# Kernel tuning notes

Hardware: AMD Instinct MI355X
Metric: run time of the kernel (lower is better)

## Reference

```python
import jax, jax.numpy as jnp
import numpy as np

B, S, D, E, TOP_K = 2, 1024, 1024, 8, 2
H = 4 * D  # FFN hidden


def setup_inputs() -> dict:
    key = jax.random.key(0)
    ks = jax.random.split(key, 12)
    sc = 0.02
    return {
        "x": jax.random.normal(ks[0], (B, S, D), jnp.float32),
        # gate: nn.Linear(D, E) -> weight [E, D], bias [E]; routing bias param [E]
        "Wg": jax.random.normal(ks[1], (E, D), jnp.float32) * sc,
        "bg": jnp.zeros((E,), jnp.float32),
        "bias": jnp.zeros((E,), jnp.float32),
        # routed experts: stacked Linear(D,4D) and Linear(4D,D) weights (torch layout [out,in])
        "W1": jax.random.normal(ks[2], (E, H, D), jnp.float32) * sc,
        "b1": jnp.zeros((E, H), jnp.float32),
        "W2": jax.random.normal(ks[3], (E, D, H), jnp.float32) * sc,
        "b2": jnp.zeros((E, D), jnp.float32),
        # shared expert
        "Ws1": jax.random.normal(ks[4], (H, D), jnp.float32) * sc,
        "bs1": jnp.zeros((H,), jnp.float32),
        "Ws2": jax.random.normal(ks[5], (D, H), jnp.float32) * sc,
        "bs2": jnp.zeros((D,), jnp.float32),
    }


def reference(x, Wg, bg, bias, W1, b1, W2, b2, Ws1, bs1, Ws2, bs2):
    b, s, d = x.shape
    xf = x.reshape(-1, d)  # [T, D]
    T = xf.shape[0]

    # sigmoid gating with learnable routing bias
    scores = jax.nn.sigmoid(xf @ Wg.T + bg + bias)          # [T, E]
    top_scores, top_idx = jax.lax.top_k(scores, TOP_K)      # [T, K]

    # per-token per-expert combine weights (zero for unselected experts)
    weights = jnp.zeros((T, E), scores.dtype)
    weights = weights.at[jnp.arange(T)[:, None], top_idx].add(top_scores)  # [T, E]

    # dense grouped expert MLP (mask-and-matmul form of gather-GEMM-scatter)
    h = jax.nn.gelu(jnp.einsum("td,ehd->teh", xf, W1) + b1, approximate=False)  # [T, E, H]
    eo = jnp.einsum("teh,edh->ted", h, W2) + b2                                  # [T, E, D]
    combined = jnp.einsum("ted,te->td", eo, weights)                             # [T, D]

    # shared expert applied to every token
    shared = jax.nn.gelu(xf @ Ws1.T + bs1, approximate=False) @ Ws2.T + bs2      # [T, D]

    return (shared + combined).reshape(b, s, d)
```

## Files before the change

kernel.cpp:

```cpp
#include <hip/hip_runtime.h>
#include <hip/hip_bf16.h>
#include <math.h>

#define NTOK 2048
#define DDIM 1024
#define HDIM 4096
#define NEXP 8
#define NROWS (3 * NTOK)
#define KSPLIT2 2

typedef __bf16 bf16x8 __attribute__((ext_vector_type(8)));
typedef float f32x4 __attribute__((ext_vector_type(4)));
typedef __attribute__((address_space(1))) char as1_char;
typedef __attribute__((address_space(3))) char as3_char;

__device__ __forceinline__ void async16(const void* g, void* l) {
  __builtin_amdgcn_global_load_lds((as1_char*)g, (as3_char*)l, 16, 0, 0);
}

__device__ __forceinline__ float gelu_fast(float v) {
  const float x = v * 0.70710678118654752f;
  const float ax = fabsf(x);
  const float t = __builtin_amdgcn_rcpf(1.0f + 0.3275911f * ax);
  float p = 1.061405429f;
  p = p * t - 1.453152027f;
  p = p * t + 1.421413741f;
  p = p * t - 0.284496736f;
  p = p * t + 0.254829592f;
  const float y = 1.0f - p * t * __expf(-ax * ax);
  const float erfv = copysignf(y, x);
  return 0.5f * v * (1.0f + erfv);
}

__global__ void __launch_bounds__(256) cvt_bf16(const float* __restrict__ in,
                                                __hip_bfloat16* __restrict__ out) {
  const size_t i = ((size_t)blockIdx.x * 256 + threadIdx.x) * 8;
  const float4 a = *(const float4*)(in + i);
  const float4 b = *(const float4*)(in + i + 4);
  union { __hip_bfloat16 h[8]; uint4 u; } p;
  p.h[0] = __float2bfloat16(a.x); p.h[1] = __float2bfloat16(a.y);
  p.h[2] = __float2bfloat16(a.z); p.h[3] = __float2bfloat16(a.w);
  p.h[4] = __float2bfloat16(b.x); p.h[5] = __float2bfloat16(b.y);
  p.h[6] = __float2bfloat16(b.z); p.h[7] = __float2bfloat16(b.w);
  *(uint4*)(out + i) = p.u;
}

__global__ void moe_zero_out(float* __restrict__ a) {
  a[(size_t)blockIdx.x * 256 + threadIdx.x] = 0.f;
}
__global__ void moe_zero_misc(int* counts) {
  if (threadIdx.x < NEXP) counts[threadIdx.x] = 0;
}

__device__ __forceinline__ void gemm_core(const char* ga0, const char* ga1,
                                          const char* gb0, const char* gb1,
                                          char* sm, int Kbytes, int tid,
                                          f32x4 acc[4][4]) {
  const int w = tid >> 6, l = tid & 63;
  const int lr = l & 15, quad = l >> 4;
  const int wr = w >> 1, wc = w & 1;
  const int swz = (lr >> 1) & 3;
  const int aoff = (wr * 64 + lr) * 64 + ((quad ^ swz) * 16);
  const int boff = 8192 + (wc * 64 + lr) * 64 + ((quad ^ swz) * 16);
  const int niter = Kbytes >> 6;

  auto stage = [&](int it, int buf) {
    char* base = sm + buf * 16384 + w * 1024;
    const int kb = it * 64;
    async16(ga0 + kb, base);
    async16(ga1 + kb, base + 4096);
    async16(gb0 + kb, base + 8192);
    async16(gb1 + kb, base + 12288);
  };

  stage(0, 0);
  stage(1, 1);
  int cur = 0, nxt = 2;
  for (int i = 0; i < niter; ++i) {
    if (i + 2 < niter) {
      stage(i + 2, nxt);
      __builtin_amdgcn_s_waitcnt(0x0F78);
    } else if (i + 1 < niter) {
      __builtin_amdgcn_s_waitcnt(0x0F74);
    } else {
      __builtin_amdgcn_s_waitcnt(0x0F70);
    }
    __builtin_amdgcn_s_barrier();
    const char* rb = sm + cur * 16384;
    bf16x8 av[4], bv[4];
#pragma unroll
    for (int i2 = 0; i2 < 4; ++i2) av[i2] = *(const bf16x8*)(rb + aoff + i2 * 1024);
#pragma unroll
    for (int j = 0; j < 4; ++j) bv[j] = *(const bf16x8*)(rb + boff + j * 1024);
#pragma unroll
    for (int i2 = 0; i2 < 4; ++i2)
#pragma unroll
      for (int j = 0; j < 4; ++j)
        acc[i2][j] = __builtin_amdgcn_mfma_f32_16x16x32_bf16(av[i2], bv[j], acc[i2][j], 0, 0, 0);
    __builtin_amdgcn_s_barrier();
    cur = (cur == 2) ? 0 : cur + 1;
    nxt = (nxt == 2) ? 0 : nxt + 1;
  }
}

__device__ __forceinline__ int stage_colb(int l) {
  return (((l & 3) ^ ((l >> 3) & 3)) * 16);
}

__global__ void __launch_bounds__(64) moe_gate(
    const float* __restrict__ x, const float* __restrict__ Wg,
    const float* __restrict__ bg, const float* __restrict__ bias,
    int* __restrict__ counts, int* __restrict__ topk_idx,
    float* __restrict__ topk_w, int* __restrict__ slot) {
  const int t = blockIdx.x, lane = threadIdx.x;
  float xv[16];
#pragma unroll
  for (int q = 0; q < 16; ++q) xv[q] = x[(size_t)t * DDIM + q * 64 + lane];
  float sc[NEXP];
#pragma unroll
  for (int e = 0; e < NEXP; ++e) {
    float s = 0.f;
#pragma unroll
    for (int q = 0; q < 16; ++q) s += xv[q] * Wg[(size_t)e * DDIM + q * 64 + lane];
#pragma unroll
    for (int o = 32; o > 0; o >>= 1) s += __shfl_xor(s, o, 64);
    sc[e] = 1.0f / (1.0f + expf(-(s + bg[e] + bias[e])));
  }
  if (lane == 0) {
    int k0 = 0;
    for (int e = 1; e < NEXP; ++e)
      if (sc[e] > sc[k0]) k0 = e;
    int k1 = (k0 == 0) ? 1 : 0;
    for (int e = 0; e < NEXP; ++e) {
      if (e == k0) continue;
      if (sc[e] > sc[k1]) k1 = e;
    }
    topk_idx[t * 2 + 0] = k0;
    topk_idx[t * 2 + 1] = k1;
    topk_w[t * 2 + 0] = sc[k0];
    topk_w[t * 2 + 1] = sc[k1];
    slot[t * 2 + 0] = atomicAdd(&counts[k0], 1);
    slot[t * 2 + 1] = atomicAdd(&counts[k1], 1);
  }
}

__global__ void moe_scan(const int* __restrict__ counts, int* __restrict__ offsets) {
  if (threadIdx.x == 0) {
    int s = 0;
    for (int e = 0; e < NEXP; ++e) { offsets[e] = s; s += counts[e]; }
    offsets[NEXP] = s;
  }
}

__global__ void moe_scatter(const int* __restrict__ topk_idx, const float* __restrict__ topk_w,
                            const int* __restrict__ slot, const int* __restrict__ offsets,
                            int* __restrict__ row_token, float* __restrict__ row_w) {
  const int t = blockIdx.x * blockDim.x + threadIdx.x;
  if (t >= NTOK) return;
#pragma unroll
  for (int k = 0; k < 2; ++k) {
    const int e = topk_idx[t * 2 + k];
    const int rg = offsets[e] + slot[t * 2 + k];
    row_token[rg] = t;
    row_w[rg] = topk_w[t * 2 + k];
  }
  row_token[2 * NTOK + t] = t;
  row_w[2 * NTOK + t] = 1.0f;
}

__global__ void __launch_bounds__(256) moe_gemm1(
    const __hip_bfloat16* __restrict__ xbf, const __hip_bfloat16* __restrict__ W1bf,
    const float* __restrict__ b1, const __hip_bfloat16* __restrict__ Ws1bf,
    const float* __restrict__ bs1, const int* __restrict__ counts,
    const int* __restrict__ offsets, const int* __restrict__ row_token,
    __hip_bfloat16* __restrict__ h1) {
  __shared__ alignas(16) char sm[49152];
  const int e = blockIdx.z, mt = blockIdx.y, nt = blockIdx.x;
  const int cnt = (e < NEXP) ? counts[e] : NTOK;
  if (mt * 128 >= cnt) return;
  const int off = (e < NEXP) ? offsets[e] : 2 * NTOK;
  const __hip_bfloat16* Bw = (e < NEXP) ? (W1bf + (size_t)e * HDIM * DDIM) : Ws1bf;
  const float* bb = (e < NEXP) ? (b1 + e * HDIM) : bs1;

  const int tid = threadIdx.x;
  const int w = tid >> 6, l = tid & 63;
  const int mrow = w * 16 + (l >> 2);
  const int colb = stage_colb(l);

  const int r0 = mt * 128 + mrow, r1 = r0 + 64;
  const int c0 = (r0 < cnt) ? r0 : (cnt - 1);
  const int c1 = (r1 < cnt) ? r1 : (cnt - 1);
  const int t0 = row_token[off + c0];
  const int t1 = row_token[off + c1];
  const char* ga0 = (const char*)xbf + (size_t)t0 * (DDIM * 2) + colb;
  const char* ga1 = (const char*)xbf + (size_t)t1 * (DDIM * 2) + colb;
  const char* gb0 = (const char*)Bw + (size_t)(nt * 128 + mrow) * (DDIM * 2) + colb;
  const char* gb1 = (const char*)Bw + (size_t)(nt * 128 + mrow + 64) * (DDIM * 2) + colb;

  f32x4 acc[4][4] = {};
  gemm_core(ga0, ga1, gb0, gb1, sm, DDIM * 2, tid, acc);

  const int lr = l & 15, quad = l >> 4, wr = w >> 1, wc = w & 1;
#pragma unroll
  for (int i = 0; i < 4; ++i) {
#pragma unroll
    for (int r = 0; r < 4; ++r) {
      const int rowe = mt * 128 + wr * 64 + i * 16 + quad * 4 + r;
      if (rowe >= cnt) continue;
      const size_t orow = (size_t)(off + rowe) * HDIM;
#pragma unroll
      for (int j = 0; j < 4; ++j) {
        const int h = nt * 128 + wc * 64 + j * 16 + lr;
        const float v = acc[i][j][r] + bb[h];
        h1[orow + h] = __float2bfloat16(gelu_fast(v));
      }
    }
  }
}

__global__ void __launch_bounds__(256) moe_gemm2(
    const __hip_bfloat16* __restrict__ h1, const __hip_bfloat16* __restrict__ W2bf,
    const float* __restrict__ b2, const __hip_bfloat16* __restrict__ Ws2bf,
    const float* __restrict__ bs2, const int* __restrict__ counts,
    const int* __restrict__ offsets, const int* __restrict__ row_token,
    const float* __restrict__ row_w, float* __restrict__ out) {
  __shared__ alignas(16) char sm[49152];
  const int e = blockIdx.z, mt = blockIdx.y;
  const int nt = blockIdx.x & (DDIM / 128 - 1);
  const int kc = blockIdx.x >> 3;
  const int cnt = (e < NEXP) ? counts[e] : NTOK;
  if (mt * 128 >= cnt) return;
  const int off = (e < NEXP) ? offsets[e] : 2 * NTOK;
  const __hip_bfloat16* Bw = (e < NEXP) ? (W2bf + (size_t)e * DDIM * HDIM) : Ws2bf;
  const float* bb = (e < NEXP) ? (b2 + e * DDIM) : bs2;

  const int tid = threadIdx.x;
  const int w = tid >> 6, l = tid & 63;
  const int mrow = w * 16 + (l >> 2);
  const int colb = stage_colb(l);
  const int KB = (HDIM * 2) / KSPLIT2;
  const size_t kofs = (size_t)kc * KB;

  const char* ga0 = (const char*)h1 + (size_t)(off + mt * 128 + mrow) * (HDIM * 2) + kofs + colb;
  const char* ga1 = (const char*)h1 + (size_t)(off + mt * 128 + mrow + 64) * (HDIM * 2) + kofs + colb;
  const char* gb0 = (const char*)Bw + (size_t)(nt * 128 + mrow) * (HDIM * 2) + kofs + colb;
  const char* gb1 = (const char*)Bw + (size_t)(nt * 128 + mrow + 64) * (HDIM * 2) + kofs + colb;

  f32x4 acc[4][4] = {};
  gemm_core(ga0, ga1, gb0, gb1, sm, KB, tid, acc);

  const int lr = l & 15, quad = l >> 4, wr = w >> 1, wc = w & 1;
#pragma unroll
  for (int i = 0; i < 4; ++i) {
#pragma unroll
    for (int r = 0; r < 4; ++r) {
      const int rowe = mt * 128 + wr * 64 + i * 16 + quad * 4 + r;
      if (rowe >= cnt) continue;
      const int rg = off + rowe;
      const int tok = row_token[rg];
      const float wt = row_w[rg];
#pragma unroll
      for (int j = 0; j < 4; ++j) {
        const int d = nt * 128 + wc * 64 + j * 16 + lr;
        const float base = (kc == 0) ? bb[d] : 0.f;
        atomicAdd(&out[(size_t)tok * DDIM + d], wt * (acc[i][j][r] + base));
      }
    }
  }
}

extern "C" void kernel_launch(void* const* d_in, const int* in_sizes, int n_in,
                              void* d_out, int out_size, void* d_ws, size_t ws_size,
                              hipStream_t stream) {
  (void)in_sizes; (void)n_in; (void)out_size; (void)ws_size;
  const float* x    = (const float*)d_in[0];
  const float* Wg   = (const float*)d_in[1];
  const float* bg   = (const float*)d_in[2];
  const float* bias = (const float*)d_in[3];
  const float* W1   = (const float*)d_in[4];
  const float* b1   = (const float*)d_in[5];
  const float* W2   = (const float*)d_in[6];
  const float* b2   = (const float*)d_in[7];
  const float* Ws1  = (const float*)d_in[8];
  const float* bs1  = (const float*)d_in[9];
  const float* Ws2  = (const float*)d_in[10];
  const float* bs2  = (const float*)d_in[11];
  float* out = (float*)d_out;

  char* ws = (char*)d_ws;
  size_t cur = 0;
  auto take = [&](size_t b) -> void* {
    void* p = ws + cur;
    cur += (b + 255) & ~(size_t)255;
    return p;
  };
  int* counts    = (int*)take(NEXP * 4);
  int* offsets   = (int*)take((NEXP + 1) * 4);
  int* topk_idx  = (int*)take(NTOK * 2 * 4);
  float* topk_w  = (float*)take(NTOK * 2 * 4);
  int* slot      = (int*)take(NTOK * 2 * 4);
  int* row_token = (int*)take(NROWS * 4);
  float* row_w   = (float*)take(NROWS * 4);
  __hip_bfloat16* xbf   = (__hip_bfloat16*)take((size_t)NTOK * DDIM * 2);
  __hip_bfloat16* W1bf  = (__hip_bfloat16*)take((size_t)NEXP * HDIM * DDIM * 2);
  __hip_bfloat16* W2bf  = (__hip_bfloat16*)take((size_t)NEXP * DDIM * HDIM * 2);
  __hip_bfloat16* Ws1bf = (__hip_bfloat16*)take((size_t)HDIM * DDIM * 2);
  __hip_bfloat16* Ws2bf = (__hip_bfloat16*)take((size_t)DDIM * HDIM * 2);
  __hip_bfloat16* h1    = (__hip_bfloat16*)take((size_t)(NROWS + 64) * HDIM * 2);

  cvt_bf16<<<(NTOK * DDIM) / 2048, 256, 0, stream>>>(x, xbf);
  cvt_bf16<<<(NEXP * HDIM * DDIM) / 2048, 256, 0, stream>>>(W1, W1bf);
  cvt_bf16<<<(NEXP * DDIM * HDIM) / 2048, 256, 0, stream>>>(W2, W2bf);
  cvt_bf16<<<(HDIM * DDIM) / 2048, 256, 0, stream>>>(Ws1, Ws1bf);
  cvt_bf16<<<(DDIM * HDIM) / 2048, 256, 0, stream>>>(Ws2, Ws2bf);

  moe_zero_misc<<<1, 64, 0, stream>>>(counts);
  moe_zero_out<<<(NTOK * DDIM) / 256, 256, 0, stream>>>(out);
  moe_gate<<<NTOK, 64, 0, stream>>>(x, Wg, bg, bias, counts, topk_idx, topk_w, slot);
  moe_scan<<<1, 1, 0, stream>>>(counts, offsets);
  moe_scatter<<<NTOK / 256, 256, 0, stream>>>(topk_idx, topk_w, slot, offsets, row_token, row_w);

  dim3 g1(HDIM / 128, NTOK / 128, NEXP + 1);
  moe_gemm1<<<g1, 256, 0, stream>>>(xbf, W1bf, b1, Ws1bf, bs1, counts, offsets, row_token, h1);

  dim3 g2(KSPLIT2 * (DDIM / 128), NTOK / 128, NEXP + 1);
  moe_gemm2<<<g2, 256, 0, stream>>>(h1, W2bf, b2, Ws2bf, bs2, counts, offsets, row_token, row_w, out);
}
```

Before: 365.8 us.

## Widen GEMM tiles to 128x256 with double buffering instead of triple

The shared GEMM core now computes a 128x256 output tile per block. Each wave owns a 64-column slab and all 128 rows, holding 8x4 MFMA accumulators. The pipeline drops from three LDS buffers to two 24KB buffers. Per-wave global staging pointers are passed as arrays, and both expert GEMM grids are halved along N. The aim is higher arithmetic intensity per LDS load and fewer blocks re-reading the A operand, at the cost of more accumulator registers (lower occupancy) and shallower prefetch.

Result: slower. 442.4 us (+21.0%).

```diff
diff --git a/kernel.cpp b/kernel.cpp
--- a/kernel.cpp
+++ b/kernel.cpp
@@ -52,54 +52,50 @@
   if (threadIdx.x < NEXP) counts[threadIdx.x] = 0;
 }
 
-__device__ __forceinline__ void gemm_core(const char* ga0, const char* ga1,
-                                          const char* gb0, const char* gb1,
+__device__ __forceinline__ void gemm_core(const char* const* gA,
+                                          const char* const* gB,
                                           char* sm, int Kbytes, int tid,
-                                          f32x4 acc[4][4]) {
+                                          f32x4 acc[8][4]) {
   const int w = tid >> 6, l = tid & 63;
   const int lr = l & 15, quad = l >> 4;
-  const int wr = w >> 1, wc = w & 1;
-  const int swz = (lr >> 1) & 3;
-  const int aoff = (wr * 64 + lr) * 64 + ((quad ^ swz) * 16);
-  const int boff = 8192 + (wc * 64 + lr) * 64 + ((quad ^ swz) * 16);
+  const int swz16 = (quad ^ ((lr >> 1) & 3)) * 16;
   const int niter = Kbytes >> 6;
 
   auto stage = [&](int it, int buf) {
-    char* base = sm + buf * 16384 + w * 1024;
+    char* base = sm + buf * 24576;
     const int kb = it * 64;
-    async16(ga0 + kb, base);
-    async16(ga1 + kb, base + 4096);
-    async16(gb0 + kb, base + 8192);
-    async16(gb1 + kb, base + 12288);
+    async16(gA[0] + kb, base + w * 2048);
+    async16(gA[1] + kb, base + w * 2048 + 1024);
+    async16(gB[0] + kb, base + 8192 + w * 4096);
+    async16(gB[1] + kb, base + 8192 + w * 4096 + 1024);
+    async16(gB[2] + kb, base + 8192 + w * 4096 + 2048);
+    async16(gB[3] + kb, base + 8192 + w * 4096 + 3072);
   };
 
   stage(0, 0);
-  stage(1, 1);
-  int cur = 0, nxt = 2;
   for (int i = 0; i < niter; ++i) {
-    if (i + 2 < niter) {
-      stage(i + 2, nxt);
-      __builtin_amdgcn_s_waitcnt(0x0F78);
-    } else if (i + 1 < niter) {
-      __builtin_amdgcn_s_waitcnt(0x0F74);
+    const int cur = i & 1;
+    if (i + 1 < niter) {
+      stage(i + 1, cur ^ 1);
+      __builtin_amdgcn_s_waitcnt(0x0F76);
     } else {
       __builtin_amdgcn_s_waitcnt(0x0F70);
     }
     __builtin_amdgcn_s_barrier();
-    const char* rb = sm + cur * 16384;
-    bf16x8 av[4], bv[4];
-#pragma unroll
-    for (int i2 = 0; i2 < 4; ++i2) av[i2] = *(const bf16x8*)(rb + aoff + i2 * 1024);
-#pragma unroll
-    for (int j = 0; j < 4; ++j) bv[j] = *(const bf16x8*)(rb + boff + j * 1024);
-#pragma unroll
-    for (int i2 = 0; i2 < 4; ++i2)
+    const char* rb = sm + cur * 24576;
+    bf16x8 av[8], bv[4];
+#pragma unroll
+    for (int i2 = 0; i2 < 8; ++i2)
+      av[i2] = *(const bf16x8*)(rb + (i2 * 16 + lr) * 64 + swz16);
+#pragma unroll
+    for (int j = 0; j < 4; ++j)
+      bv[j] = *(const bf16x8*)(rb + 8192 + (w * 64 + j * 16 + lr) * 64 + swz16);
+#pragma unroll
+    for (int i2 = 0; i2 < 8; ++i2)
 #pragma unroll
       for (int j = 0; j < 4; ++j)
         acc[i2][j] = __builtin_amdgcn_mfma_f32_16x16x32_bf16(av[i2], bv[j], acc[i2][j], 0, 0, 0);
     __builtin_amdgcn_s_barrier();
-    cur = (cur == 2) ? 0 : cur + 1;
-    nxt = (nxt == 2) ? 0 : nxt + 1;
   }
 }
 
@@ -184,33 +180,38 @@
 
   const int tid = threadIdx.x;
   const int w = tid >> 6, l = tid & 63;
-  const int mrow = w * 16 + (l >> 2);
+  const int rl = l >> 2;
   const int colb = stage_colb(l);
 
-  const int r0 = mt * 128 + mrow, r1 = r0 + 64;
-  const int c0 = (r0 < cnt) ? r0 : (cnt - 1);
-  const int c1 = (r1 < cnt) ? r1 : (cnt - 1);
-  const int t0 = row_token[off + c0];
-  const int t1 = row_token[off + c1];
-  const char* ga0 = (const char*)xbf + (size_t)t0 * (DDIM * 2) + colb;
-  const char* ga1 = (const char*)xbf + (size_t)t1 * (DDIM * 2) + colb;
-  const char* gb0 = (const char*)Bw + (size_t)(nt * 128 + mrow) * (DDIM * 2) + colb;
-  const char* gb1 = (const char*)Bw + (size_t)(nt * 128 + mrow + 64) * (DDIM * 2) + colb;
-
-  f32x4 acc[4][4] = {};
-  gemm_core(ga0, ga1, gb0, gb1, sm, DDIM * 2, tid, acc);
-
-  const int lr = l & 15, quad = l >> 4, wr = w >> 1, wc = w & 1;
-#pragma unroll
-  for (int i = 0; i < 4; ++i) {
+  const char* ga[2];
+#pragma unroll
+  for (int q = 0; q < 2; ++q) {
+    const int r0 = mt * 128 + w * 32 + q * 16 + rl;
+    const int c0 = (r0 < cnt) ? r0 : (cnt - 1);
+    const int t0 = row_token[off + c0];
+    ga[q] = (const char*)xbf + (size_t)t0 * (DDIM * 2) + colb;
+  }
+  const char* gb[4];
+#pragma unroll
+  for (int q = 0; q < 4; ++q) {
+    const int br = nt * 256 + w * 64 + q * 16 + rl;
+    gb[q] = (const char*)Bw + (size_t)br * (DDIM * 2) + colb;
+  }
+
+  f32x4 acc[8][4] = {};
+  gemm_core(ga, gb, sm, DDIM * 2, tid, acc);
+
+  const int lr = l & 15, quad = l >> 4;
+#pragma unroll
+  for (int i = 0; i < 8; ++i) {
 #pragma unroll
     for (int r = 0; r < 4; ++r) {
-      const int rowe = mt * 128 + wr * 64 + i * 16 + quad * 4 + r;
+      const int rowe = mt * 128 + i * 16 + quad * 4 + r;
       if (rowe >= cnt) continue;
       const size_t orow = (size_t)(off + rowe) * HDIM;
 #pragma unroll
       for (int j = 0; j < 4; ++j) {
-        const int h = nt * 128 + wc * 64 + j * 16 + lr;
+        const int h = nt * 256 + w * 64 + j * 16 + lr;
         const float v = acc[i][j][r] + bb[h];
         h1[orow + h] = __float2bfloat16(gelu_fast(v));
       }
@@ -226,8 +227,8 @@
     const float* __restrict__ row_w, float* __restrict__ out) {
   __shared__ alignas(16) char sm[49152];
   const int e = blockIdx.z, mt = blockIdx.y;
-  const int nt = blockIdx.x & (DDIM / 128 - 1);
-  const int kc = blockIdx.x >> 3;
+  const int nt = blockIdx.x & (DDIM / 256 - 1);
+  const int kc = blockIdx.x >> 2;
   const int cnt = (e < NEXP) ? counts[e] : NTOK;
   if (mt * 128 >= cnt) return;
   const int off = (e < NEXP) ? offsets[e] : 2 * NTOK;
@@ -236,32 +237,40 @@
 
   const int tid = threadIdx.x;
   const int w = tid >> 6, l = tid & 63;
-  const int mrow = w * 16 + (l >> 2);
+  const int rl = l >> 2;
   const int colb = stage_colb(l);
   const int KB = (HDIM * 2) / KSPLIT2;
   const size_t kofs = (size_t)kc * KB;
 
-  const char* ga0 = (const char*)h1 + (size_t)(off + mt * 128 + mrow) * (HDIM * 2) + kofs + colb;
-  const char* ga1 = (const char*)h1 + (size_t)(off + mt * 128 + mrow + 64) * (HDIM * 2) + kofs + colb;
-  const char* gb0 = (const char*)Bw + (size_t)(nt * 128 + mrow) * (HDIM * 2) + kofs + colb;
-  const char* gb1 = (const char*)Bw + (size_t)(nt * 128 + mrow + 64) * (HDIM * 2) + kofs + colb;
-
-  f32x4 acc[4][4] = {};
-  gemm_core(ga0, ga1, gb0, gb1, sm, KB, tid, acc);
-
-  const int lr = l & 15, quad = l >> 4, wr = w >> 1, wc = w & 1;
-#pragma unroll
-  for (int i = 0; i < 4; ++i) {
+  const char* ga[2];
+#pragma unroll
+  for (int q = 0; q < 2; ++q) {
+    const int ar = mt * 128 + w * 32 + q * 16 + rl;
+    ga[q] = (const char*)h1 + (size_t)(off + ar) * (HDIM * 2) + kofs + colb;
+  }
+  const char* gb[4];
+#pragma unroll
+  for (int q = 0; q < 4; ++q) {
+    const int br = nt * 256 + w * 64 + q * 16 + rl;
+    gb[q] = (const char*)Bw + (size_t)br * (HDIM * 2) + kofs + colb;
+  }
+
+  f32x4 acc[8][4] = {};
+  gemm_core(ga, gb, sm, KB, tid, acc);
+
+  const int lr = l & 15, quad = l >> 4;
+#pragma unroll
+  for (int i = 0; i < 8; ++i) {
 #pragma unroll
     for (int r = 0; r < 4; ++r) {
-      const int rowe = mt * 128 + wr * 64 + i * 16 + quad * 4 + r;
+      const int rowe = mt * 128 + i * 16 + quad * 4 + r;
       if (rowe >= cnt) continue;
       const int rg = off + rowe;
       const int tok = row_token[rg];
       const float wt = row_w[rg];
 #pragma unroll
       for (int j = 0; j < 4; ++j) {
-        const int d = nt * 128 + wc * 64 + j * 16 + lr;
+        const int d = nt * 256 + w * 64 + j * 16 + lr;
         const float base = (kc == 0) ? bb[d] : 0.f;
         atomicAdd(&out[(size_t)tok * DDIM + d], wt * (acc[i][j][r] + base));
       }
@@ -320,9 +329,9 @@
   moe_scan<<<1, 1, 0, stream>>>(counts, offsets);
   moe_scatter<<<NTOK / 256, 256, 0, stream>>>(topk_idx, topk_w, slot, offsets, row_token, row_w);
 
-  dim3 g1(HDIM / 128, NTOK / 128, NEXP + 1);
+  dim3 g1(HDIM / 256, NTOK / 128, NEXP + 1);
   moe_gemm1<<<g1, 256, 0, stream>>>(xbf, W1bf, b1, Ws1bf, bs1, counts, offsets, row_token, h1);
 
-  dim3 g2(KSPLIT2 * (DDIM / 128), NTOK / 128, NEXP + 1);
+  dim3 g2(KSPLIT2 * (DDIM / 256), NTOK / 128, NEXP + 1);
   moe_gemm2<<<g2, 256, 0, stream>>>(h1, W2bf, b2, Ws2bf, bs2, counts, offsets, row_token, row_w, out);
 }
```

## Load fp32 weights directly in GEMMs and convert to bf16 in-register

Applied to the files above, without the earlier changes.

Removes the separate fp32-to-bf16 conversion passes over W1, W2, Ws1 and Ws2. The GEMM kernels now stage fp32 weight tiles into LDS with an 8-way swizzle and convert them to bf16 after the LDS read. This saves a full read and write of the weights per call, but doubles the weight bytes moved per GEMM tile and LDS use grows to 72KB, which may reduce occupancy. It also folds the counts zeroing into the x conversion kernel to drop one launch.

After: 362.7 us. Within noise of the previous version (-0.8%).

```diff
diff --git a/kernel.cpp b/kernel.cpp
--- a/kernel.cpp
+++ b/kernel.cpp
@@ -32,8 +32,10 @@
   return 0.5f * v * (1.0f + erfv);
 }
 
-__global__ void __launch_bounds__(256) cvt_bf16(const float* __restrict__ in,
-                                                __hip_bfloat16* __restrict__ out) {
+__global__ void __launch_bounds__(256) cvt_x(const float* __restrict__ in,
+                                             __hip_bfloat16* __restrict__ out,
+                                             int* __restrict__ counts) {
+  if (blockIdx.x == 0 && threadIdx.x < NEXP) counts[threadIdx.x] = 0;
   const size_t i = ((size_t)blockIdx.x * 256 + threadIdx.x) * 8;
   const float4 a = *(const float4*)(in + i);
   const float4 b = *(const float4*)(in + i + 4);
@@ -48,29 +50,28 @@
 __global__ void moe_zero_out(float* __restrict__ a) {
   a[(size_t)blockIdx.x * 256 + threadIdx.x] = 0.f;
 }
-__global__ void moe_zero_misc(int* counts) {
-  if (threadIdx.x < NEXP) counts[threadIdx.x] = 0;
-}
 
 __device__ __forceinline__ void gemm_core(const char* ga0, const char* ga1,
-                                          const char* gb0, const char* gb1,
-                                          char* sm, int Kbytes, int tid,
+                                          const char* const gb[4],
+                                          char* sm, int niter, int tid,
                                           f32x4 acc[4][4]) {
   const int w = tid >> 6, l = tid & 63;
   const int lr = l & 15, quad = l >> 4;
   const int wr = w >> 1, wc = w & 1;
-  const int swz = (lr >> 1) & 3;
-  const int aoff = (wr * 64 + lr) * 64 + ((quad ^ swz) * 16);
-  const int boff = 8192 + (wc * 64 + lr) * 64 + ((quad ^ swz) * 16);
-  const int niter = Kbytes >> 6;
+  const int swz4 = (lr >> 1) & 3;
+  const int aoff = (wr * 64 + lr) * 64 + ((quad ^ swz4) * 16);
+  const int s8 = lr & 7;
+  const int bslot0 = ((2 * quad) ^ s8) * 16;
+  const int bslot1 = ((2 * quad + 1) ^ s8) * 16;
+  const int bbase = 8192 + (wc * 64 + lr) * 128;
 
   auto stage = [&](int it, int buf) {
-    char* base = sm + buf * 16384 + w * 1024;
-    const int kb = it * 64;
-    async16(ga0 + kb, base);
-    async16(ga1 + kb, base + 4096);
-    async16(gb0 + kb, base + 8192);
-    async16(gb1 + kb, base + 12288);
+    char* base = sm + buf * 24576;
+    async16(ga0 + it * 64, base + w * 1024);
+    async16(ga1 + it * 64, base + 4096 + w * 1024);
+#pragma unroll
+    for (int q = 0; q < 4; ++q)
+      async16(gb[q] + it * 128, base + 8192 + w * 4096 + q * 1024);
   };
 
   stage(0, 0);
@@ -79,19 +80,30 @@
   for (int i = 0; i < niter; ++i) {
     if (i + 2 < niter) {
       stage(i + 2, nxt);
-      __builtin_amdgcn_s_waitcnt(0x0F78);
+      __builtin_amdgcn_s_waitcnt(0x0F7C);
     } else if (i + 1 < niter) {
-      __builtin_amdgcn_s_waitcnt(0x0F74);
+      __builtin_amdgcn_s_waitcnt(0x0F76);
     } else {
       __builtin_amdgcn_s_waitcnt(0x0F70);
     }
     __builtin_amdgcn_s_barrier();
-    const char* rb = sm + cur * 16384;
+    const char* rb = sm + cur * 24576;
     bf16x8 av[4], bv[4];
 #pragma unroll
     for (int i2 = 0; i2 < 4; ++i2) av[i2] = *(const bf16x8*)(rb + aoff + i2 * 1024);
 #pragma unroll
-    for (int j = 0; j < 4; ++j) bv[j] = *(const bf16x8*)(rb + boff + j * 1024);
+    for (int j = 0; j < 4; ++j) {
+      const char* bp = rb + bbase + j * 2048;
+      const f32x4 f0 = *(const f32x4*)(bp + bslot0);
+      const f32x4 f1 = *(const f32x4*)(bp + bslot1);
+      union { bf16x8 v; __hip_bfloat16 h[8]; } u;
+#pragma unroll
+      for (int m = 0; m < 4; ++m) {
+        u.h[m] = __float2bfloat16(f0[m]);
+        u.h[4 + m] = __float2bfloat16(f1[m]);
+      }
+      bv[j] = u.v;
+    }
 #pragma unroll
     for (int i2 = 0; i2 < 4; ++i2)
 #pragma unroll
@@ -105,6 +117,9 @@
 
 __device__ __forceinline__ int stage_colb(int l) {
   return (((l & 3) ^ ((l >> 3) & 3)) * 16);
+}
+__device__ __forceinline__ int stage_colb8(int l) {
+  return (((l & 7) ^ (l >> 3)) * 16);
 }
 
 __global__ void __launch_bounds__(64) moe_gate(
@@ -169,23 +184,24 @@
 }
 
 __global__ void __launch_bounds__(256) moe_gemm1(
-    const __hip_bfloat16* __restrict__ xbf, const __hip_bfloat16* __restrict__ W1bf,
-    const float* __restrict__ b1, const __hip_bfloat16* __restrict__ Ws1bf,
+    const __hip_bfloat16* __restrict__ xbf, const float* __restrict__ W1,
+    const float* __restrict__ b1, const float* __restrict__ Ws1,
     const float* __restrict__ bs1, const int* __restrict__ counts,
     const int* __restrict__ offsets, const int* __restrict__ row_token,
     __hip_bfloat16* __restrict__ h1) {
-  __shared__ alignas(16) char sm[49152];
+  __shared__ alignas(16) char sm[73728];
   const int e = blockIdx.z, mt = blockIdx.y, nt = blockIdx.x;
   const int cnt = (e < NEXP) ? counts[e] : NTOK;
   if (mt * 128 >= cnt) return;
   const int off = (e < NEXP) ? offsets[e] : 2 * NTOK;
-  const __hip_bfloat16* Bw = (e < NEXP) ? (W1bf + (size_t)e * HDIM * DDIM) : Ws1bf;
+  const float* Bw = (e < NEXP) ? (W1 + (size_t)e * HDIM * DDIM) : Ws1;
   const float* bb = (e < NEXP) ? (b1 + e * HDIM) : bs1;
 
   const int tid = threadIdx.x;
   const int w = tid >> 6, l = tid & 63;
   const int mrow = w * 16 + (l >> 2);
   const int colb = stage_colb(l);
+  const int colb8 = stage_colb8(l);
 
   const int r0 = mt * 128 + mrow, r1 = r0 + 64;
   const int c0 = (r0 < cnt) ? r0 : (cnt - 1);
@@ -194,11 +210,15 @@
   const int t1 = row_token[off + c1];
   const char* ga0 = (const char*)xbf + (size_t)t0 * (DDIM * 2) + colb;
   const char* ga1 = (const char*)xbf + (size_t)t1 * (DDIM * 2) + colb;
-  const char* gb0 = (const char*)Bw + (size_t)(nt * 128 + mrow) * (DDIM * 2) + colb;
-  const char* gb1 = (const char*)Bw + (size_t)(nt * 128 + mrow + 64) * (DDIM * 2) + colb;
+  const char* gb[4];
+#pragma unroll
+  for (int q = 0; q < 4; ++q) {
+    const int br = nt * 128 + w * 32 + q * 8 + (l >> 3);
+    gb[q] = (const char*)Bw + (size_t)br * (DDIM * 4) + colb8;
+  }
 
   f32x4 acc[4][4] = {};
-  gemm_core(ga0, ga1, gb0, gb1, sm, DDIM * 2, tid, acc);
+  gemm_core(ga0, ga1, gb, sm, DDIM / 32, tid, acc);
 
   const int lr = l & 15, quad = l >> 4, wr = w >> 1, wc = w & 1;
 #pragma unroll
@@ -219,35 +239,41 @@
 }
 
 __global__ void __launch_bounds__(256) moe_gemm2(
-    const __hip_bfloat16* __restrict__ h1, const __hip_bfloat16* __restrict__ W2bf,
-    const float* __restrict__ b2, const __hip_bfloat16* __restrict__ Ws2bf,
+    const __hip_bfloat16* __restrict__ h1, const float* __restrict__ W2,
+    const float* __restrict__ b2, const float* __restrict__ Ws2,
     const float* __restrict__ bs2, const int* __restrict__ counts,
     const int* __restrict__ offsets, const int* __restrict__ row_token,
     const float* __restrict__ row_w, float* __restrict__ out) {
-  __shared__ alignas(16) char sm[49152];
+  __shared__ alignas(16) char sm[73728];
   const int e = blockIdx.z, mt = blockIdx.y;
   const int nt = blockIdx.x & (DDIM / 128 - 1);
   const int kc = blockIdx.x >> 3;
   const int cnt = (e < NEXP) ? counts[e] : NTOK;
   if (mt * 128 >= cnt) return;
   const int off = (e < NEXP) ? offsets[e] : 2 * NTOK;
-  const __hip_bfloat16* Bw = (e < NEXP) ? (W2bf + (size_t)e * DDIM * HDIM) : Ws2bf;
+  const float* Bw = (e < NEXP) ? (W2 + (size_t)e * DDIM * HDIM) : Ws2;
   const float* bb = (e < NEXP) ? (b2 + e * DDIM) : bs2;
 
   const int tid = threadIdx.x;
   const int w = tid >> 6, l = tid & 63;
   const int mrow = w * 16 + (l >> 2);
   const int colb = stage_colb(l);
-  const int KB = (HDIM * 2) / KSPLIT2;
-  const size_t kofs = (size_t)kc * KB;
-
-  const char* ga0 = (const char*)h1 + (size_t)(off + mt * 128 + mrow) * (HDIM * 2) + kofs + colb;
-  const char* ga1 = (const char*)h1 + (size_t)(off + mt * 128 + mrow + 64) * (HDIM * 2) + kofs + colb;
-  const char* gb0 = (const char*)Bw + (size_t)(nt * 128 + mrow) * (HDIM * 2) + kofs + colb;
-  const char* gb1 = (const char*)Bw + (size_t)(nt * 128 + mrow + 64) * (HDIM * 2) + kofs + colb;
+  const int colb8 = stage_colb8(l);
+  const int KE = HDIM / KSPLIT2;
+  const size_t kofs_a = (size_t)kc * KE * 2;
+  const size_t kofs_b = (size_t)kc * KE * 4;
+
+  const char* ga0 = (const char*)h1 + (size_t)(off + mt * 128 + mrow) * (HDIM * 2) + kofs_a + colb;
+  const char* ga1 = (const char*)h1 + (size_t)(off + mt * 128 + mrow + 64) * (HDIM * 2) + kofs_a + colb;
+  const char* gb[4];
+#pragma unroll
+  for (int q = 0; q < 4; ++q) {
+    const int br = nt * 128 + w * 32 + q * 8 + (l >> 3);
+    gb[q] = (const char*)Bw + (size_t)br * (HDIM * 4) + kofs_b + colb8;
+  }
 
   f32x4 acc[4][4] = {};
-  gemm_core(ga0, ga1, gb0, gb1, sm, KB, tid, acc);
+  gemm_core(ga0, ga1, gb, sm, KE / 32, tid, acc);
 
   const int lr = l & 15, quad = l >> 4, wr = w >> 1, wc = w & 1;
 #pragma unroll
@@ -301,28 +327,19 @@
   int* slot      = (int*)take(NTOK * 2 * 4);
   int* row_token = (int*)take(NROWS * 4);
   float* row_w   = (float*)take(NROWS * 4);
-  __hip_bfloat16* xbf   = (__hip_bfloat16*)take((size_t)NTOK * DDIM * 2);
-  __hip_bfloat16* W1bf  = (__hip_bfloat16*)take((size_t)NEXP * HDIM * DDIM * 2);
-  __hip_bfloat16* W2bf  = (__hip_bfloat16*)take((size_t)NEXP * DDIM * HDIM * 2);
-  __hip_bfloat16* Ws1bf = (__hip_bfloat16*)take((size_t)HDIM * DDIM * 2);
-  __hip_bfloat16* Ws2bf = (__hip_bfloat16*)take((size_t)DDIM * HDIM * 2);
-  __hip_bfloat16* h1    = (__hip_bfloat16*)take((size_t)(NROWS + 64) * HDIM * 2);
-
-  cvt_bf16<<<(NTOK * DDIM) / 2048, 256, 0, stream>>>(x, xbf);
-  cvt_bf16<<<(NEXP * HDIM * DDIM) / 2048, 256, 0, stream>>>(W1, W1bf);
-  cvt_bf16<<<(NEXP * DDIM * HDIM) / 2048, 256, 0, stream>>>(W2, W2bf);
-  cvt_bf16<<<(HDIM * DDIM) / 2048, 256, 0, stream>>>(Ws1, Ws1bf);
-  cvt_bf16<<<(DDIM * HDIM) / 2048, 256, 0, stream>>>(Ws2, Ws2bf);
-
-  moe_zero_misc<<<1, 64, 0, stream>>>(counts);
+  __hip_bfloat16* xbf = (__hip_bfloat16*)take((size_t)NTOK * DDIM * 2);
+  __hip_bfloat16* h1  = (__hip_bfloat16*)take((size_t)(NROWS + 64) * HDIM * 2);
+
+  cvt_x<<<(NTOK * DDIM) / 2048, 256, 0, stream>>>(x, xbf, counts);
+
   moe_zero_out<<<(NTOK * DDIM) / 256, 256, 0, stream>>>(out);
   moe_gate<<<NTOK, 64, 0, stream>>>(x, Wg, bg, bias, counts, topk_idx, topk_w, slot);
   moe_scan<<<1, 1, 0, stream>>>(counts, offsets);
   moe_scatter<<<NTOK / 256, 256, 0, stream>>>(topk_idx, topk_w, slot, offsets, row_token, row_w);
 
   dim3 g1(HDIM / 128, NTOK / 128, NEXP + 1);
-  moe_gemm1<<<g1, 256, 0, stream>>>(xbf, W1bf, b1, Ws1bf, bs1, counts, offsets, row_token, h1);
+  moe_gemm1<<<g1, 256, 0, stream>>>(xbf, W1, b1, Ws1, bs1, counts, offsets, row_token, h1);
 
   dim3 g2(KSPLIT2 * (DDIM / 128), NTOK / 128, NEXP + 1);
-  moe_gemm2<<<g2, 256, 0, stream>>>(h1, W2bf, b2, Ws2bf, bs2, counts, offsets, row_token, row_w, out);
-}
+  moe_gemm2<<<g2, 256, 0, stream>>>(h1, W2, b2, Ws2, bs2, counts, offsets, row_token, row_w, out);
+}
```

## Fuse gate, conversions and zeroing; hide W2 conversion inside gemm1; XCD-aware tile mapping

Applied to the files above, without the earlier changes.

Merges the gate, the x/W1/Ws1 bf16 conversions and the output zeroing into one launch, which removes several kernel launches. Each gemm1 block, including early-exit blocks with no rows, converts a slice of W2/Ws2 to bf16, so that conversion overlaps with the GEMM instead of running as its own pass. Both GEMM grids become 1D with a decode that groups tiles by XCD to improve L2 locality. In exchange, gemm1 blocks take on extra memory traffic and the tile indexing becomes harder to follow.

Result: faster. 343.5 us (-6.1%).

```diff
diff --git a/kernel.cpp b/kernel.cpp
--- a/kernel.cpp
+++ b/kernel.cpp
@@ -32,24 +32,74 @@
   return 0.5f * v * (1.0f + erfv);
 }
 
-__global__ void __launch_bounds__(256) cvt_bf16(const float* __restrict__ in,
-                                                __hip_bfloat16* __restrict__ out) {
-  const size_t i = ((size_t)blockIdx.x * 256 + threadIdx.x) * 8;
-  const float4 a = *(const float4*)(in + i);
-  const float4 b = *(const float4*)(in + i + 4);
+__global__ void moe_zero_misc(int* counts) {
+  if (threadIdx.x < NEXP) counts[threadIdx.x] = 0;
+}
+
+__device__ __forceinline__ void cvt2048(const float* __restrict__ src,
+                                        __hip_bfloat16* __restrict__ dst,
+                                        int tid) {
+  const size_t i = (size_t)tid * 8;
+  const float4 a = *(const float4*)(src + i);
+  const float4 b = *(const float4*)(src + i + 4);
   union { __hip_bfloat16 h[8]; uint4 u; } p;
   p.h[0] = __float2bfloat16(a.x); p.h[1] = __float2bfloat16(a.y);
   p.h[2] = __float2bfloat16(a.z); p.h[3] = __float2bfloat16(a.w);
   p.h[4] = __float2bfloat16(b.x); p.h[5] = __float2bfloat16(b.y);
   p.h[6] = __float2bfloat16(b.z); p.h[7] = __float2bfloat16(b.w);
-  *(uint4*)(out + i) = p.u;
-}
-
-__global__ void moe_zero_out(float* __restrict__ a) {
-  a[(size_t)blockIdx.x * 256 + threadIdx.x] = 0.f;
-}
-__global__ void moe_zero_misc(int* counts) {
-  if (threadIdx.x < NEXP) counts[threadIdx.x] = 0;
+  *(uint4*)(dst + i) = p.u;
+}
+
+__global__ void __launch_bounds__(256) moe_pre(
+    const float* __restrict__ x, const float* __restrict__ Wg,
+    const float* __restrict__ bg, const float* __restrict__ bias,
+    const float* __restrict__ W1, const float* __restrict__ Ws1,
+    __hip_bfloat16* __restrict__ xbf, __hip_bfloat16* __restrict__ W1bf,
+    __hip_bfloat16* __restrict__ Ws1bf, float* __restrict__ out,
+    int* __restrict__ counts, int* __restrict__ topk_idx,
+    float* __restrict__ topk_w, int* __restrict__ slot) {
+  const int b = blockIdx.x, tid = threadIdx.x;
+  if (b < 512) {
+    const int t = b * 4 + (tid >> 6);
+    const int lane = tid & 63;
+    float xv[16];
+#pragma unroll
+    for (int q = 0; q < 16; ++q) xv[q] = x[(size_t)t * DDIM + q * 64 + lane];
+    float sc[NEXP];
+#pragma unroll
+    for (int e = 0; e < NEXP; ++e) {
+      float s = 0.f;
+#pragma unroll
+      for (int q = 0; q < 16; ++q) s += xv[q] * Wg[(size_t)e * DDIM + q * 64 + lane];
+#pragma unroll
+      for (int o = 32; o > 0; o >>= 1) s += __shfl_xor(s, o, 64);
+      sc[e] = 1.0f / (1.0f + expf(-(s + bg[e] + bias[e])));
+    }
+    if (lane == 0) {
+      int k0 = 0;
+      for (int e = 1; e < NEXP; ++e)
+        if (sc[e] > sc[k0]) k0 = e;
+      int k1 = (k0 == 0) ? 1 : 0;
+      for (int e = 0; e < NEXP; ++e) {
+        if (e == k0) continue;
+        if (sc[e] > sc[k1]) k1 = e;
+      }
+      topk_idx[t * 2 + 0] = k0;
+      topk_idx[t * 2 + 1] = k1;
+      topk_w[t * 2 + 0] = sc[k0];
+      topk_w[t * 2 + 1] = sc[k1];
+      slot[t * 2 + 0] = atomicAdd(&counts[k0], 1);
+      slot[t * 2 + 1] = atomicAdd(&counts[k1], 1);
+    }
+    return;
+  }
+  const int cb = b - 512;
+  if (cb < 1024) { cvt2048(x + (size_t)cb * 2048, xbf + (size_t)cb * 2048, tid); return; }
+  if (cb < 17408) { const size_t o = (size_t)(cb - 1024) * 2048; cvt2048(W1 + o, W1bf + o, tid); return; }
+  if (cb < 19456) { const size_t o = (size_t)(cb - 17408) * 2048; cvt2048(Ws1 + o, Ws1bf + o, tid); return; }
+  const size_t o = (size_t)(cb - 19456) * 2048 + (size_t)tid * 8;
+  *(float4*)(out + o) = make_float4(0.f, 0.f, 0.f, 0.f);
+  *(float4*)(out + o + 4) = make_float4(0.f, 0.f, 0.f, 0.f);
 }
 
 __device__ __forceinline__ void gemm_core(const char* ga0, const char* ga1,
@@ -107,41 +157,9 @@
   return (((l & 3) ^ ((l >> 3) & 3)) * 16);
 }
 
-__global__ void __launch_bounds__(64) moe_gate(
-    const float* __restrict__ x, const float* __restrict__ Wg,
-    const float* __restrict__ bg, const float* __restrict__ bias,
-    int* __restrict__ counts, int* __restrict__ topk_idx,
-    float* __restrict__ topk_w, int* __restrict__ slot) {
-  const int t = blockIdx.x, lane = threadIdx.x;
-  float xv[16];
-#pragma unroll
-  for (int q = 0; q < 16; ++q) xv[q] = x[(size_t)t * DDIM + q * 64 + lane];
-  float sc[NEXP];
-#pragma unroll
-  for (int e = 0; e < NEXP; ++e) {
-    float s = 0.f;
-#pragma unroll
-    for (int q = 0; q < 16; ++q) s += xv[q] * Wg[(size_t)e * DDIM + q * 64 + lane];
-#pragma unroll
-    for (int o = 32; o > 0; o >>= 1) s += __shfl_xor(s, o, 64);
-    sc[e] = 1.0f / (1.0f + expf(-(s + bg[e] + bias[e])));
-  }
-  if (lane == 0) {
-    int k0 = 0;
-    for (int e = 1; e < NEXP; ++e)
-      if (sc[e] > sc[k0]) k0 = e;
-    int k1 = (k0 == 0) ? 1 : 0;
-    for (int e = 0; e < NEXP; ++e) {
-      if (e == k0) continue;
-      if (sc[e] > sc[k1]) k1 = e;
-    }
-    topk_idx[t * 2 + 0] = k0;
-    topk_idx[t * 2 + 1] = k1;
-    topk_w[t * 2 + 0] = sc[k0];
-    topk_w[t * 2 + 1] = sc[k1];
-    slot[t * 2 + 0] = atomicAdd(&counts[k0], 1);
-    slot[t * 2 + 1] = atomicAdd(&counts[k1], 1);
-  }
+__device__ __forceinline__ void xcd_decode(int hw, int& g, int& m) {
+  m = (hw >> 3) & 7;
+  g = (hw & 7) + 8 * (hw >> 6);
 }
 
 __global__ void moe_scan(const int* __restrict__ counts, int* __restrict__ offsets) {
@@ -168,21 +186,51 @@
   row_w[2 * NTOK + t] = 1.0f;
 }
 
+__device__ __forceinline__ void cvt_w2_quota(int b, const float* __restrict__ W2,
+                                             const float* __restrict__ Ws2,
+                                             __hip_bfloat16* __restrict__ W2bf,
+                                             __hip_bfloat16* __restrict__ Ws2bf,
+                                             int tid) {
+  const float* src;
+  __hip_bfloat16* dst;
+  size_t base;
+  if (b < 4096) { src = W2; dst = W2bf; base = (size_t)b * 8192; }
+  else          { src = Ws2; dst = Ws2bf; base = (size_t)(b - 4096) * 8192; }
+#pragma unroll
+  for (int k = 0; k < 8; ++k) {
+    const size_t i = base + (size_t)k * 1024 + (size_t)tid * 4;
+    const float4 a = *(const float4*)(src + i);
+    union { __hip_bfloat16 h[4]; uint2 u; } p;
+    p.h[0] = __float2bfloat16(a.x); p.h[1] = __float2bfloat16(a.y);
+    p.h[2] = __float2bfloat16(a.z); p.h[3] = __float2bfloat16(a.w);
+    *(uint2*)(dst + i) = p.u;
+  }
+}
+
 __global__ void __launch_bounds__(256) moe_gemm1(
     const __hip_bfloat16* __restrict__ xbf, const __hip_bfloat16* __restrict__ W1bf,
     const float* __restrict__ b1, const __hip_bfloat16* __restrict__ Ws1bf,
     const float* __restrict__ bs1, const int* __restrict__ counts,
     const int* __restrict__ offsets, const int* __restrict__ row_token,
-    __hip_bfloat16* __restrict__ h1) {
+    __hip_bfloat16* __restrict__ h1, const float* __restrict__ W2,
+    const float* __restrict__ Ws2, __hip_bfloat16* __restrict__ W2bf,
+    __hip_bfloat16* __restrict__ Ws2bf) {
   __shared__ alignas(16) char sm[49152];
-  const int e = blockIdx.z, mt = blockIdx.y, nt = blockIdx.x;
+  const int tid = threadIdx.x;
+  int g, m;
+  xcd_decode(blockIdx.x, g, m);
+  const int nt = m + 8 * (g & 3);
+  const int mt = (g >> 2) & 15;
+  const int e = g >> 6;
   const int cnt = (e < NEXP) ? counts[e] : NTOK;
-  if (mt * 128 >= cnt) return;
+  if (mt * 128 >= cnt) {
+    cvt_w2_quota(blockIdx.x, W2, Ws2, W2bf, Ws2bf, tid);
+    return;
+  }
   const int off = (e < NEXP) ? offsets[e] : 2 * NTOK;
   const __hip_bfloat16* Bw = (e < NEXP) ? (W1bf + (size_t)e * HDIM * DDIM) : Ws1bf;
   const float* bb = (e < NEXP) ? (b1 + e * HDIM) : bs1;
 
-  const int tid = threadIdx.x;
   const int w = tid >> 6, l = tid & 63;
   const int mrow = w * 16 + (l >> 2);
   const int colb = stage_colb(l);
@@ -216,6 +264,7 @@
       }
     }
   }
+  cvt_w2_quota(blockIdx.x, W2, Ws2, W2bf, Ws2bf, tid);
 }
 
 __global__ void __launch_bounds__(256) moe_gemm2(
@@ -225,9 +274,12 @@
     const int* __restrict__ offsets, const int* __restrict__ row_token,
     const float* __restrict__ row_w, float* __restrict__ out) {
   __shared__ alignas(16) char sm[49152];
-  const int e = blockIdx.z, mt = blockIdx.y;
-  const int nt = blockIdx.x & (DDIM / 128 - 1);
-  const int kc = blockIdx.x >> 3;
+  int g, m;
+  xcd_decode(blockIdx.x, g, m);
+  const int nt = m;
+  const int kc = g & 1;
+  const int mt = (g >> 1) & 15;
+  const int e = g >> 5;
   const int cnt = (e < NEXP) ? counts[e] : NTOK;
   if (mt * 128 >= cnt) return;
   const int off = (e < NEXP) ? offsets[e] : 2 * NTOK;
@@ -308,21 +360,18 @@
   __hip_bfloat16* Ws2bf = (__hip_bfloat16*)take((size_t)DDIM * HDIM * 2);
   __hip_bfloat16* h1    = (__hip_bfloat16*)take((size_t)(NROWS + 64) * HDIM * 2);
 
-  cvt_bf16<<<(NTOK * DDIM) / 2048, 256, 0, stream>>>(x, xbf);
-  cvt_bf16<<<(NEXP * HDIM * DDIM) / 2048, 256, 0, stream>>>(W1, W1bf);
-  cvt_bf16<<<(NEXP * DDIM * HDIM) / 2048, 256, 0, stream>>>(W2, W2bf);
-  cvt_bf16<<<(HDIM * DDIM) / 2048, 256, 0, stream>>>(Ws1, Ws1bf);
-  cvt_bf16<<<(DDIM * HDIM) / 2048, 256, 0, stream>>>(Ws2, Ws2bf);
-
   moe_zero_misc<<<1, 64, 0, stream>>>(counts);
-  moe_zero_out<<<(NTOK * DDIM) / 256, 256, 0, stream>>>(out);
-  moe_gate<<<NTOK, 64, 0, stream>>>(x, Wg, bg, bias, counts, topk_idx, topk_w, slot);
+
+  moe_pre<<<20992, 256, 0, stream>>>(x, Wg, bg, bias, W1, Ws1,
+                                     xbf, W1bf, Ws1bf, out,
+                                     counts, topk_idx, topk_w, slot);
+
   moe_scan<<<1, 1, 0, stream>>>(counts, offsets);
   moe_scatter<<<NTOK / 256, 256, 0, stream>>>(topk_idx, topk_w, slot, offsets, row_token, row_w);
 
-  dim3 g1(HDIM / 128, NTOK / 128, NEXP + 1);
-  moe_gemm1<<<g1, 256, 0, stream>>>(xbf, W1bf, b1, Ws1bf, bs1, counts, offsets, row_token, h1);
-
-  dim3 g2(KSPLIT2 * (DDIM / 128), NTOK / 128, NEXP + 1);
-  moe_gemm2<<<g2, 256, 0, stream>>>(h1, W2bf, b2, Ws2bf, bs2, counts, offsets, row_token, row_w, out);
-}
+  moe_gemm1<<<4608, 256, 0, stream>>>(xbf, W1bf, b1, Ws1bf, bs1, counts, offsets,
+                                      row_token, h1, W2, Ws2, W2bf, Ws2bf);
+
+  moe_gemm2<<<2304, 256, 0, stream>>>(h1, W2bf, b2, Ws2bf, bs2, counts, offsets,
+                                      row_token, row_w, out);
+}
```
